# Optimization experiments

Measured on AMD Instinct MI355X. Metric: run time of the kernel, lower is better.

## Reference

```python
import jax, jax.numpy as jnp
import numpy as np

BATCH, C_IN, T, V = 32, 192, 256, 21
HEADS, C_OUT = 3, 192
NEG_SLOPE = 0.2


def setup_inputs() -> dict:
    key = jax.random.key(0)
    k1, k2, k3, k4, k5 = jax.random.split(key, 5)
    x = jax.random.normal(k1, (BATCH, C_IN, T, V), dtype=jnp.float32)
    # adjacency: 0/1 entries, diagonal forced to 1 so every softmax row is valid
    A = (jax.random.uniform(k2, (HEADS, V, V)) > 0.5).astype(jnp.float32)
    d = jnp.arange(V)
    A = A.at[:, d, d].set(1.0)
    W_proj = jax.random.normal(k3, (HEADS * C_OUT, C_IN), dtype=jnp.float32) * 0.05
    score_src = jax.random.normal(k4, (1, HEADS, C_OUT), dtype=jnp.float32) * 0.1
    score_tgt = jax.random.normal(k5, (1, HEADS, C_OUT), dtype=jnp.float32) * 0.1
    return {"x": x, "A": A, "W_proj": W_proj, "score_src": score_src, "score_tgt": score_tgt}


def reference(x, A, W_proj, score_src, score_tgt):
    batch, c_in, t, v = x.shape  # v == 21
    # (b, c, t, v) -> (b, t, v, c); dropout is identity in eval mode
    xp = jnp.transpose(x, (0, 2, 3, 1))
    # linear projection (no bias): (N, heads, C)
    proj = (xp.reshape(-1, c_in) @ W_proj.T).reshape(-1, HEADS, C_OUT)
    N = proj.shape[0]
    Bp = N // v  # = batch * t
    # additive attention scores, reduced over feature dim
    ss = jnp.sum(proj * score_src, axis=-1, keepdims=True)  # (N, H, 1)
    st = jnp.sum(proj * score_tgt, axis=-1, keepdims=True)  # (N, H, 1)
    ss = ss.reshape(Bp, v, HEADS, 1).transpose(0, 2, 1, 3)  # (Bp, H, V, 1)
    st = st.reshape(Bp, v, HEADS, 1).transpose(0, 2, 3, 1)  # (Bp, H, 1, V)
    scores = jax.nn.leaky_relu(ss + st, negative_slope=NEG_SLOPE)  # (Bp, H, V, V)
    # mask zero adjacency entries with -inf, then masked softmax over neighbors
    A_masked = jnp.where(A == 0.0, -jnp.inf, A)  # (H, V, V)
    attn = jax.nn.softmax(scores + A_masked, axis=-1)  # (Bp, H, V, V)
    # aggregate neighbor features per head
    nf = proj.reshape(Bp, v, HEADS, C_OUT).transpose(0, 2, 1, 3)  # (Bp, H, V, C)
    out = jnp.einsum('bhij,bhjc->bhic', attn, nf)  # (Bp, H, V, C)
    # faithful to torch: flatten (Bp*H*V, C) then regroup consecutive triples
    out = out.reshape(-1, 3, C_OUT)  # (N, 3, C)
    # skip connection (last dims always equal) then mean over dim 1
    out = out + proj
    out = out.mean(axis=1)  # (N, C)
    # faithful to torch: raw view back to (batch, C, t, v) (reinterpret, not transpose)
    out = out.reshape(batch, C_OUT, t, v)
    return out
```

## Files before the change

### kernel.cpp

```cpp
#include <hip/hip_runtime.h>
#include <stdint.h>

#define BATCH 32
#define C_IN 192
#define T_DIM 256
#define V_N 21
#define HEADS 3
#define C_OUTD 192
#define NPROJ 576
#define NEG_SLOPE 0.2f
#define W_ELEMS (NPROJ * C_IN)
#define WF_BLOCKS 432

typedef __attribute__((ext_vector_type(8))) short short8;
typedef __attribute__((ext_vector_type(4))) float f32x4;

#define XS_LD 200
#define PROJB_LD 600
#define PROJB_BYTES (21 * PROJB_LD * 2)
#define ATTN2_OFF 25216
#define ATTN2_LD 40
#define SS_OFF (ATTN2_OFF + HEADS * 16 * ATTN2_LD * 2)
#define LDS_TOTAL (SS_OFF + 512)

__device__ __forceinline__ unsigned short f2bf(float f) {
    uint32_t u = __float_as_uint(f);
    u += 0x7fffu + ((u >> 16) & 1u);
    return (unsigned short)(u >> 16);
}
__device__ __forceinline__ float bf2f(unsigned short h) {
    return __uint_as_float(((uint32_t)h) << 16);
}

__global__ void convert_kernel(const float* __restrict__ W,
                               const float* __restrict__ ssrc,
                               const float* __restrict__ stgt,
                               unsigned short* __restrict__ Wf) {
    if (blockIdx.x < WF_BLOCKS) {
        int o = blockIdx.x * 256 + threadIdx.x;
        int j    = o & 7;
        int lane = (o >> 3) & 63;
        int p    = o >> 9;
        int ks   = p % 6;
        int nt   = p / 6;
        int n = nt * 16 + (lane & 15);
        int k = ks * 32 + (lane >> 4) * 8 + j;
        Wf[o] = f2bf(W[n * C_IN + k]);
    } else {
        int h = blockIdx.x - WF_BLOCKS;
        int k = threadIdx.x;
        if (k < C_IN) {
            float ws = 0.f, wt = 0.f;
#pragma unroll 4
            for (int co = 0; co < C_OUTD; co++) {
                float w = W[(h * C_OUTD + co) * C_IN + k];
                ws += w * ssrc[h * C_OUTD + co];
                wt += w * stgt[h * C_OUTD + co];
            }
            int ks = k >> 5;
            int r  = (k >> 3) & 3;
            int j  = k & 7;
            Wf[(((36 * 6 + ks) * 64) + r * 16 + h) * 8 + j]     = f2bf(ws);
            Wf[(((36 * 6 + ks) * 64) + r * 16 + 3 + h) * 8 + j] = f2bf(wt);
        }
    }
}

__global__ __launch_bounds__(256)
void gat_fused_kernel(const float* __restrict__ x,
                      const float* __restrict__ A,
                      const unsigned short* __restrict__ Wf,
                      float* __restrict__ out) {
    __shared__ __align__(16) char lds[LDS_TOTAL];
    unsigned short* xs    = (unsigned short*)lds;
    unsigned short* projb = (unsigned short*)lds;
    unsigned short* attn2 = (unsigned short*)(lds + ATTN2_OFF);
    float* ssl = (float*)(lds + SS_OFF);
    float* stl = (float*)(lds + SS_OFF + 256);

    const int tid  = threadIdx.x;
    const int wv   = tid >> 6;
    const int lane = tid & 63;
    const int q    = lane >> 4;
    const int l15  = lane & 15;
    const int bp   = blockIdx.x;
    const int b    = bp >> 8;
    const int t    = bp & 255;

    const float* xb = x + (size_t)b * (C_IN * T_DIM * V_N) + (size_t)t * V_N;
    if (tid < 252) {
        int c0 = tid / 21;
        int v  = tid - c0 * 21;
        const float* p = xb + (size_t)c0 * (T_DIM * V_N) + v;
        float xr[16];
#pragma unroll
        for (int k = 0; k < 16; k++) xr[k] = p[(size_t)k * (12 * T_DIM * V_N)];
        unsigned short* xrow = xs + v * XS_LD + c0;
#pragma unroll
        for (int k = 0; k < 16; k++) xrow[12 * k] = f2bf(xr[k]);
    }
    __syncthreads();

    f32x4 acc[9][2];
#pragma unroll
    for (int nt = 0; nt < 9; nt++)
#pragma unroll
        for (int mt = 0; mt < 2; mt++)
            acc[nt][mt] = (f32x4){0.f, 0.f, 0.f, 0.f};

    const int colbase = wv * 144 + l15;
    const unsigned short* wf0 = Wf + ((size_t)(wv * 9) * 6) * 512 + lane * 8;
#pragma unroll
    for (int ks = 0; ks < 6; ks++) {
        const int koff = ks * 32 + q * 8;
        short8 a0 = *(const short8*)(xs + l15 * XS_LD + koff);
        short8 a1 = *(const short8*)(xs + (16 + l15) * XS_LD + koff);
#pragma unroll
        for (int nt = 0; nt < 9; nt++) {
            short8 bfr = *(const short8*)(wf0 + (nt * 6 + ks) * 512);
            acc[nt][0] = __builtin_amdgcn_mfma_f32_16x16x32_bf16(a0, bfr, acc[nt][0], 0, 0, 0);
            acc[nt][1] = __builtin_amdgcn_mfma_f32_16x16x32_bf16(a1, bfr, acc[nt][1], 0, 0, 0);
        }
    }

    if (wv == 3) {
        f32x4 as0 = (f32x4){0.f, 0.f, 0.f, 0.f};
        f32x4 as1 = (f32x4){0.f, 0.f, 0.f, 0.f};
        const unsigned short* wfs = Wf + (size_t)(36 * 6) * 512 + lane * 8;
#pragma unroll
        for (int ks = 0; ks < 6; ks++) {
            const int koff = ks * 32 + q * 8;
            short8 a0 = *(const short8*)(xs + l15 * XS_LD + koff);
            short8 a1 = *(const short8*)(xs + (16 + l15) * XS_LD + koff);
            short8 bs = *(const short8*)(wfs + ks * 512);
            as0 = __builtin_amdgcn_mfma_f32_16x16x32_bf16(a0, bs, as0, 0, 0, 0);
            as1 = __builtin_amdgcn_mfma_f32_16x16x32_bf16(a1, bs, as1, 0, 0, 0);
        }
        if (l15 < 6) {
            float* dst = (l15 < 3) ? ssl : stl;
            int h = (l15 < 3) ? l15 : l15 - 3;
#pragma unroll
            for (int r = 0; r < 4; r++) {
                int v0 = q * 4 + r;
                dst[v0 * 3 + h] = as0[r];
                int v1 = 16 + q * 4 + r;
                if (v1 < 21) dst[v1 * 3 + h] = as1[r];
            }
        }
    }
    __syncthreads();

#pragma unroll
    for (int nt = 0; nt < 9; nt++) {
        const int col = colbase + nt * 16;
#pragma unroll
        for (int r = 0; r < 4; r++) {
            int row0 = q * 4 + r;
            projb[row0 * PROJB_LD + col] = f2bf(acc[nt][0][r]);
            int row1 = 16 + q * 4 + r;
            if (row1 < 21) projb[row1 * PROJB_LD + col] = f2bf(acc[nt][1][r]);
        }
    }

    if (wv < 3 && lane < 21) {
        const int h = wv, i = lane;
        const float* Ah = A + (h * 21 + i) * 21;
        float si = ssl[i * 3 + h];
        float vals[21];
        float mx = -1e30f;
#pragma unroll
        for (int j = 0; j < 21; j++) {
            float a = Ah[j];
            float z = si + stl[j * 3 + h];
            float e = (z > 0.f) ? z : NEG_SLOPE * z;
            float val = (a != 0.f) ? (e + a) : -1e30f;
            vals[j] = val;
            mx = fmaxf(mx, val);
        }
        float sum = 0.f;
#pragma unroll
        for (int j = 0; j < 21; j++) {
            float e = __expf(vals[j] - mx);
            vals[j] = e;
            sum += e;
        }
        float inv = 1.f / sum;
        int m = i / 3;
        bool wr = (i == m * 3);
        unsigned short* drow = attn2 + (h * 16 + m) * ATTN2_LD;
#pragma unroll
        for (int j = 0; j < 21; j++) {
            float vv = vals[j] * inv;
            float s = vv + __shfl_down(vv, 1) + __shfl_down(vv, 2);
            if (wr) drow[j] = f2bf(s);
        }
        if (wr) {
#pragma unroll
            for (int j = 21; j < 32; j++) drow[j] = 0;
        }
    }
    __syncthreads();

    float* outb = out + (size_t)bp * (V_N * C_OUTD);
    int rw[8];
#pragma unroll
    for (int j = 0; j < 8; j++) {
        int row = q * 8 + j;
        rw[j] = ((row > 20) ? 20 : row) * PROJB_LD;
    }
#pragma unroll
    for (int i = 0; i < 9; i++) {
        int p = wv * 9 + i;
        int h = p / 12;
        int nt = p - h * 12;
        int colh = nt * 16 + l15;
        int col = h * C_OUTD + colh;
        short8 bfr;
#pragma unroll
        for (int j = 0; j < 8; j++) bfr[j] = (short)projb[rw[j] + col];
        short8 av = *(const short8*)(attn2 + (h * 16 + l15) * ATTN2_LD + q * 8);
        f32x4 z = (f32x4){0.f, 0.f, 0.f, 0.f};
        f32x4 d = __builtin_amdgcn_mfma_f32_16x16x32_bf16(av, bfr, z, 0, 0, 0);
#pragma unroll
        for (int r = 0; r < 4; r++) {
            int m = q * 4 + r;
            if (m < 7) {
                int k = h * 7 + m;
                float skip = bf2f(projb[k * PROJB_LD + colh])
                           + bf2f(projb[k * PROJB_LD + C_OUTD + colh])
                           + bf2f(projb[k * PROJB_LD + 2 * C_OUTD + colh]);
                outb[k * C_OUTD + colh] = (d[r] + skip) * (1.f / 3.f);
            }
        }
    }
}

extern "C" void kernel_launch(void* const* d_in, const int* in_sizes, int n_in,
                              void* d_out, int out_size, void* d_ws, size_t ws_size,
                              hipStream_t stream) {
    (void)in_sizes; (void)n_in; (void)out_size; (void)ws_size;
    const float* x    = (const float*)d_in[0];
    const float* A    = (const float*)d_in[1];
    const float* W    = (const float*)d_in[2];
    const float* ssrc = (const float*)d_in[3];
    const float* stgt = (const float*)d_in[4];
    float* out = (float*)d_out;
    unsigned short* Wf = (unsigned short*)d_ws;

    convert_kernel<<<WF_BLOCKS + HEADS, 256, 0, stream>>>(W, ssrc, stgt, Wf);
    gat_fused_kernel<<<BATCH * T_DIM, 256, 0, stream>>>(x, A, Wf, out);
}
```

Before: 525.5 us.

## Double block size to 512 threads, splitting projection M-tiles across waves

Raises the fused kernel from 4 to 8 waves per block. Each wave now computes one 16-row M tile instead of two, and the x load and the aggregation loop are spread over the extra waves. This is meant to raise parallelism and latency hiding and to cut per-wave register pressure. In exchange, each wave reloads the same W fragments, so weight traffic from L2 doubles, and the second M tile is mostly padding (rows 21-31).

New measurement: 466.8 us. -11.2%, faster.

```diff
diff --git a/kernel.cpp b/kernel.cpp
--- a/kernel.cpp
+++ b/kernel.cpp
@@ -66,7 +66,7 @@
     }
 }
 
-__global__ __launch_bounds__(256)
+__global__ __launch_bounds__(512)
 void gat_fused_kernel(const float* __restrict__ x,
                       const float* __restrict__ A,
                       const unsigned short* __restrict__ Wf,
@@ -83,68 +83,60 @@
     const int lane = tid & 63;
     const int q    = lane >> 4;
     const int l15  = lane & 15;
+    const int wn   = wv & 3;
+    const int wm   = wv >> 2;
     const int bp   = blockIdx.x;
     const int b    = bp >> 8;
     const int t    = bp & 255;
 
     const float* xb = x + (size_t)b * (C_IN * T_DIM * V_N) + (size_t)t * V_N;
-    if (tid < 252) {
+    if (tid < 504) {
         int c0 = tid / 21;
         int v  = tid - c0 * 21;
         const float* p = xb + (size_t)c0 * (T_DIM * V_N) + v;
-        float xr[16];
-#pragma unroll
-        for (int k = 0; k < 16; k++) xr[k] = p[(size_t)k * (12 * T_DIM * V_N)];
+        float xr[8];
+#pragma unroll
+        for (int k = 0; k < 8; k++) xr[k] = p[(size_t)k * (24 * T_DIM * V_N)];
         unsigned short* xrow = xs + v * XS_LD + c0;
 #pragma unroll
-        for (int k = 0; k < 16; k++) xrow[12 * k] = f2bf(xr[k]);
+        for (int k = 0; k < 8; k++) xrow[24 * k] = f2bf(xr[k]);
     }
     __syncthreads();
 
-    f32x4 acc[9][2];
-#pragma unroll
-    for (int nt = 0; nt < 9; nt++)
-#pragma unroll
-        for (int mt = 0; mt < 2; mt++)
-            acc[nt][mt] = (f32x4){0.f, 0.f, 0.f, 0.f};
-
-    const int colbase = wv * 144 + l15;
-    const unsigned short* wf0 = Wf + ((size_t)(wv * 9) * 6) * 512 + lane * 8;
+    f32x4 acc[9];
+#pragma unroll
+    for (int nt = 0; nt < 9; nt++) acc[nt] = (f32x4){0.f, 0.f, 0.f, 0.f};
+
+    const int colbase = wn * 144 + l15;
+    const int arow = (wm * 16 + l15) * XS_LD;
+    const unsigned short* wf0 = Wf + ((size_t)(wn * 9) * 6) * 512 + lane * 8;
 #pragma unroll
     for (int ks = 0; ks < 6; ks++) {
         const int koff = ks * 32 + q * 8;
-        short8 a0 = *(const short8*)(xs + l15 * XS_LD + koff);
-        short8 a1 = *(const short8*)(xs + (16 + l15) * XS_LD + koff);
+        short8 a = *(const short8*)(xs + arow + koff);
 #pragma unroll
         for (int nt = 0; nt < 9; nt++) {
             short8 bfr = *(const short8*)(wf0 + (nt * 6 + ks) * 512);
-            acc[nt][0] = __builtin_amdgcn_mfma_f32_16x16x32_bf16(a0, bfr, acc[nt][0], 0, 0, 0);
-            acc[nt][1] = __builtin_amdgcn_mfma_f32_16x16x32_bf16(a1, bfr, acc[nt][1], 0, 0, 0);
-        }
-    }
-
-    if (wv == 3) {
-        f32x4 as0 = (f32x4){0.f, 0.f, 0.f, 0.f};
-        f32x4 as1 = (f32x4){0.f, 0.f, 0.f, 0.f};
+            acc[nt] = __builtin_amdgcn_mfma_f32_16x16x32_bf16(a, bfr, acc[nt], 0, 0, 0);
+        }
+    }
+
+    if (wv == 3 || wv == 7) {
+        f32x4 as = (f32x4){0.f, 0.f, 0.f, 0.f};
         const unsigned short* wfs = Wf + (size_t)(36 * 6) * 512 + lane * 8;
 #pragma unroll
         for (int ks = 0; ks < 6; ks++) {
-            const int koff = ks * 32 + q * 8;
-            short8 a0 = *(const short8*)(xs + l15 * XS_LD + koff);
-            short8 a1 = *(const short8*)(xs + (16 + l15) * XS_LD + koff);
+            short8 a = *(const short8*)(xs + arow + ks * 32 + q * 8);
             short8 bs = *(const short8*)(wfs + ks * 512);
-            as0 = __builtin_amdgcn_mfma_f32_16x16x32_bf16(a0, bs, as0, 0, 0, 0);
-            as1 = __builtin_amdgcn_mfma_f32_16x16x32_bf16(a1, bs, as1, 0, 0, 0);
+            as = __builtin_amdgcn_mfma_f32_16x16x32_bf16(a, bs, as, 0, 0, 0);
         }
         if (l15 < 6) {
             float* dst = (l15 < 3) ? ssl : stl;
             int h = (l15 < 3) ? l15 : l15 - 3;
 #pragma unroll
             for (int r = 0; r < 4; r++) {
-                int v0 = q * 4 + r;
-                dst[v0 * 3 + h] = as0[r];
-                int v1 = 16 + q * 4 + r;
-                if (v1 < 21) dst[v1 * 3 + h] = as1[r];
+                int v0 = wm * 16 + q * 4 + r;
+                if (v0 < 21) dst[v0 * 3 + h] = as[r];
             }
         }
     }
@@ -155,10 +147,8 @@
         const int col = colbase + nt * 16;
 #pragma unroll
         for (int r = 0; r < 4; r++) {
-            int row0 = q * 4 + r;
-            projb[row0 * PROJB_LD + col] = f2bf(acc[nt][0][r]);
-            int row1 = 16 + q * 4 + r;
-            if (row1 < 21) projb[row1 * PROJB_LD + col] = f2bf(acc[nt][1][r]);
+            int row = wm * 16 + q * 4 + r;
+            if (row < 21) projb[row * PROJB_LD + col] = f2bf(acc[nt][r]);
         }
     }
 
@@ -209,27 +199,29 @@
         rw[j] = ((row > 20) ? 20 : row) * PROJB_LD;
     }
 #pragma unroll
-    for (int i = 0; i < 9; i++) {
-        int p = wv * 9 + i;
-        int h = p / 12;
-        int nt = p - h * 12;
-        int colh = nt * 16 + l15;
-        int col = h * C_OUTD + colh;
-        short8 bfr;
-#pragma unroll
-        for (int j = 0; j < 8; j++) bfr[j] = (short)projb[rw[j] + col];
-        short8 av = *(const short8*)(attn2 + (h * 16 + l15) * ATTN2_LD + q * 8);
-        f32x4 z = (f32x4){0.f, 0.f, 0.f, 0.f};
-        f32x4 d = __builtin_amdgcn_mfma_f32_16x16x32_bf16(av, bfr, z, 0, 0, 0);
-#pragma unroll
-        for (int r = 0; r < 4; r++) {
-            int m = q * 4 + r;
-            if (m < 7) {
-                int k = h * 7 + m;
-                float skip = bf2f(projb[k * PROJB_LD + colh])
-                           + bf2f(projb[k * PROJB_LD + C_OUTD + colh])
-                           + bf2f(projb[k * PROJB_LD + 2 * C_OUTD + colh]);
-                outb[k * C_OUTD + colh] = (d[r] + skip) * (1.f / 3.f);
+    for (int i = 0; i < 5; i++) {
+        int p = wv + 8 * i;
+        if (p < 36) {
+            int h = p / 12;
+            int nt = p - h * 12;
+            int colh = nt * 16 + l15;
+            int col = h * C_OUTD + colh;
+            short8 bfr;
+#pragma unroll
+            for (int j = 0; j < 8; j++) bfr[j] = (short)projb[rw[j] + col];
+            short8 av = *(const short8*)(attn2 + (h * 16 + l15) * ATTN2_LD + q * 8);
+            f32x4 z = (f32x4){0.f, 0.f, 0.f, 0.f};
+            f32x4 d = __builtin_amdgcn_mfma_f32_16x16x32_bf16(av, bfr, z, 0, 0, 0);
+#pragma unroll
+            for (int r = 0; r < 4; r++) {
+                int m = q * 4 + r;
+                if (m < 7) {
+                    int k = h * 7 + m;
+                    float skip = bf2f(projb[k * PROJB_LD + colh])
+                               + bf2f(projb[k * PROJB_LD + C_OUTD + colh])
+                               + bf2f(projb[k * PROJB_LD + 2 * C_OUTD + colh]);
+                    outb[k * C_OUTD + colh] = (d[r] + skip) * (1.f / 3.f);
+                }
             }
         }
     }
@@ -248,5 +240,5 @@
     unsigned short* Wf = (unsigned short*)d_ws;
 
     convert_kernel<<<WF_BLOCKS + HEADS, 256, 0, stream>>>(W, ssrc, stgt, Wf);
-    gat_fused_kernel<<<BATCH * T_DIM, 256, 0, stream>>>(x, A, Wf, out);
-}
+    gat_fused_kernel<<<BATCH * T_DIM, 512, 0, stream>>>(x, A, Wf, out);
+}
```
